# Kernel optimization log

Measured on AMD Instinct MI355X. Metric: run time of the kernel, lower is better.

## Reference

```python
import jax, jax.numpy as jnp
import numpy as np

N_CLOUDS = 16
N_PTS = 2048
K = 5            # spline kernel_size per dim
KC = K ** 3      # 125 kernel weights
BITS = np.array([[i & 1, (i >> 1) & 1, (i >> 2) & 1] for i in range(8)])  # degree-1 B-spline corners


def _radius_edges_np(pos, batch, r, max_nb=32):
    # brute-force radius graph, up to max_nb nearest neighbors within r, no self loops
    srcs, tgts = [], []
    for c in np.unique(batch):
        ids = np.where(batch == c)[0]
        P = pos[ids]
        D = np.linalg.norm(P[:, None, :] - P[None, :, :], axis=-1).astype(np.float32)
        np.fill_diagonal(D, np.inf)
        D[D > r] = np.inf
        order = np.argsort(D, axis=1)[:, :max_nb]
        valid = np.isfinite(np.take_along_axis(D, order, axis=1))
        tgt_loc = np.broadcast_to(np.arange(len(ids))[:, None], order.shape)
        srcs.append(ids[order[valid]])
        tgts.append(ids[tgt_loc[valid]])
    return np.concatenate(srcs).astype(np.int32), np.concatenate(tgts).astype(np.int32)


def _fps_np(pos, batch, ratio):
    out = []
    for c in np.unique(batch):
        ids = np.where(batch == c)[0]
        P = pos[ids]
        m = int(round(ratio * len(ids)))
        sel = [0]
        d = np.linalg.norm(P - P[0], axis=1)
        for _ in range(m - 1):
            i = int(d.argmax())
            sel.append(i)
            d = np.minimum(d, np.linalg.norm(P - P[i], axis=1))
        out.append(ids[np.array(sel)])
    return np.concatenate(out).astype(np.int32)


def setup_inputs() -> dict:
    rng = np.random.default_rng(0)
    pos = rng.random((N_CLOUDS * N_PTS, 3)).astype(np.float32)
    batch = np.repeat(np.arange(N_CLOUDS), N_PTS).astype(np.int32)

    src1, tgt1 = _radius_edges_np(pos, batch, 0.2)
    idx1 = _fps_np(pos, batch, 0.5)
    pos2, batch2 = pos[idx1], batch[idx1]
    src2, tgt2 = _radius_edges_np(pos2, batch2, 0.4)
    idx2 = _fps_np(pos2, batch2, 0.25)
    pos3, batch3 = pos2[idx2], batch2[idx2]
    src3, tgt3 = _radius_edges_np(pos3, batch3, 1.0)

    def p(shape, scale=0.1):
        return (rng.standard_normal(shape) * scale).astype(np.float32)

    inp = {
        'pos': jnp.asarray(pos), 'batch': jnp.asarray(batch),
        'src1': jnp.asarray(src1), 'tgt1': jnp.asarray(tgt1),
        'src2': jnp.asarray(src2), 'tgt2': jnp.asarray(tgt2),
        'src3': jnp.asarray(src3), 'tgt3': jnp.asarray(tgt3),
        'idx1': jnp.asarray(idx1), 'idx2': jnp.asarray(idx2),
        'W1': jnp.asarray(p((KC, 1, 64))),  'R1': jnp.asarray(p((1, 64))),   'b1': jnp.zeros((64,), jnp.float32),
        'W2': jnp.asarray(p((KC, 64, 64))), 'R2': jnp.asarray(p((64, 64))),  'b2': jnp.zeros((64,), jnp.float32),
        'W3': jnp.asarray(p((KC, 64, 128))),'R3': jnp.asarray(p((64, 128))), 'b3': jnp.zeros((128,), jnp.float32),
        'lw1': jnp.asarray(p((128, 256))), 'lb1': jnp.zeros((256,), jnp.float32),
        'lw2': jnp.asarray(p((256, 256))), 'lb2': jnp.zeros((256,), jnp.float32),
        'lw3': jnp.asarray(p((256, 10))),  'lb3': jnp.zeros((10,), jnp.float32),
    }
    return inp


def _pseudo(pos, src, tgt, r):
    return jnp.clip((pos[tgt] - pos[src]) / (2.0 * r) + 0.5, 0.0, 1.0)


def _spline_conv(x, pseudo, src, tgt, n, W, R, b):
    # SplineConv: degree-1 open B-spline basis, mean aggregation, root weight + bias
    Cin = x.shape[1]
    v = pseudo * (K - 1)                  # [E,3]
    bot = jnp.floor(v)
    frac = v - bot                        # [E,3]
    boti = bot.astype(jnp.int32)
    xj = x[src]                           # [E,Cin]
    A = jnp.zeros((n * KC, Cin), x.dtype)
    for s in range(8):                    # 8 nonzero basis products per edge
        bits = BITS[s]
        w = jnp.where(bits == 1, frac, 1.0 - frac).prod(-1)     # [E]
        idx = jnp.clip(boti + bits, 0, K - 1)                   # [E,3]
        wi = idx[:, 0] + K * idx[:, 1] + K * K * idx[:, 2]      # [E]
        A = A.at[tgt * KC + wi].add(w[:, None] * xj)
    A = A.reshape(n, KC, Cin)             # per-node per-kernel accumulated features
    msg = jnp.einsum('nkc,kco->no', A, W)
    deg = jax.ops.segment_sum(jnp.ones(tgt.shape[0], x.dtype), tgt, num_segments=n)
    msg = msg / jnp.maximum(deg, 1.0)[:, None]
    return msg + x @ R + b


def reference(pos, batch, src1, tgt1, src2, tgt2, src3, tgt3, idx1, idx2,
              W1, R1, b1, W2, R2, b2, W3, R3, b3,
              lw1, lb1, lw2, lb2, lw3, lb3):
    n1 = pos.shape[0]
    x = jnp.ones((n1, 1), pos.dtype)
    x = jax.nn.elu(_spline_conv(x, _pseudo(pos, src1, tgt1, 0.2), src1, tgt1, n1, W1, R1, b1))
    x, pos2 = x[idx1], pos[idx1]
    n2 = pos2.shape[0]
    x = jax.nn.elu(_spline_conv(x, _pseudo(pos2, src2, tgt2, 0.4), src2, tgt2, n2, W2, R2, b2))
    x, pos3 = x[idx2], pos2[idx2]
    n3 = pos3.shape[0]
    x = jax.nn.elu(_spline_conv(x, _pseudo(pos3, src3, tgt3, 1.0), src3, tgt3, n3, W3, R3, b3))
    batch3 = batch[idx1][idx2]
    num = jax.ops.segment_sum(x, batch3, num_segments=N_CLOUDS)
    cnt = jax.ops.segment_sum(jnp.ones(n3, x.dtype), batch3, num_segments=N_CLOUDS)
    g = num / jnp.maximum(cnt, 1.0)[:, None]          # global_mean_pool [16,128]
    h = jax.nn.elu(g @ lw1 + lb1)
    h = jax.nn.elu(h @ lw2 + lb2)
    # dropout is identity in eval mode
    logits = h @ lw3 + lb3
    return jax.nn.log_softmax(logits, axis=-1)
```

## Files before the change

kernel.cpp:

```cpp
#include <hip/hip_runtime.h>
#include <hip/hip_bf16.h>
#include <math.h>

#define KDIM 5
#define KC 125
#define KPAD 8192
#define EPB 32
#define NSPLIT 4
#define LDA 72
#define SSTR 40
#define XSTR 40
#define H1STR 40
#define MAXCHUNK 8192

typedef short bf16x8 __attribute__((ext_vector_type(8)));
typedef float f32x4 __attribute__((ext_vector_type(4)));

__device__ __forceinline__ float elu_f(float x) { return x > 0.f ? x : (expf(x) - 1.f); }

__device__ __forceinline__ void fadd_atomic(float* p, float v) {
    unsafeAtomicAdd(p, v);
}

__device__ __forceinline__ unsigned short f2bf(float x) {
    union { float f; unsigned u; } v; v.f = x;
    unsigned r = (v.u + 0x7FFFu + ((v.u >> 16) & 1u)) >> 16;
    return (unsigned short)r;
}

__device__ __forceinline__ void rowptr_seg(const int* __restrict__ tgt, int E, int n,
                                           int* __restrict__ rowptr, int e)
{
    if (e < E) {
        int t = tgt[e];
        int p = (e == 0) ? -1 : tgt[e - 1];
        for (int v = p + 1; v <= t; v++) rowptr[v] = e;
    } else {
        int p = tgt[E - 1];
        for (int v = p + 1; v <= n; v++) rowptr[v] = E;
    }
}

__device__ __forceinline__ void slots_seg(const float* __restrict__ posL,
                                          const int* __restrict__ src,
                                          const int* __restrict__ tgt, float rinv2,
                                          int sinkrow, unsigned* __restrict__ slots, int e)
{
    int s = src[e], t = tgt[e];
    float p0 = fminf(fmaxf((posL[t*3+0] - posL[s*3+0]) * rinv2 + 0.5f, 0.f), 1.f);
    float p1 = fminf(fmaxf((posL[t*3+1] - posL[s*3+1]) * rinv2 + 0.5f, 0.f), 1.f);
    float p2 = fminf(fmaxf((posL[t*3+2] - posL[s*3+2]) * rinv2 + 0.5f, 0.f), 1.f);
    float v0 = p0 * (KDIM - 1), v1 = p1 * (KDIM - 1), v2 = p2 * (KDIM - 1);
    int b0 = (int)floorf(v0), b1 = (int)floorf(v1), b2 = (int)floorf(v2);
    float f0 = v0 - (float)b0, f1 = v1 - (float)b1, f2 = v2 - (float)b2;
    unsigned out[8];
    #pragma unroll
    for (int sb = 0; sb < 8; sb++) {
        int i0 = sb & 1, i1 = (sb >> 1) & 1, i2 = (sb >> 2) & 1;
        float w = (i0 ? f0 : 1.f - f0) * (i1 ? f1 : 1.f - f1) * (i2 ? f2 : 1.f - f2);
        int k0 = min(b0 + i0, KDIM - 1), k1 = min(b1 + i1, KDIM - 1), k2 = min(b2 + i2, KDIM - 1);
        int wi = k0 + KDIM * k1 + KDIM * KDIM * k2;
        if (w == 0.f) wi = sinkrow;
        out[sb] = (__float_as_uint(w) & ~127u) | (unsigned)wi;
    }
    uint4* dst = (uint4*)&slots[(size_t)e * 8];
    dst[0] = make_uint4(out[0], out[1], out[2], out[3]);
    dst[1] = make_uint4(out[4], out[5], out[6], out[7]);
}

__global__ void pre1_kernel(const float* __restrict__ pos, const int* __restrict__ idx1,
                            const int* __restrict__ idx2, int n2, int n3,
                            float* __restrict__ pos2, float* __restrict__ pos3,
                            float* __restrict__ gz )
{
    int i = blockIdx.x * blockDim.x + threadIdx.x;
    int w0 = n2 * 3, w1 = w0 + n3 * 3, w2 = w1 + 16 * 128 + 16;
    if (i < w0) {
        int r = i / 3, d = i - r * 3;
        pos2[i] = pos[idx1[r] * 3 + d];
    } else if (i < w1) {
        int j = i - w0;
        int r = j / 3, d = j - r * 3;
        pos3[j] = pos[idx1[idx2[r]] * 3 + d];
    } else if (i < w2) {
        gz[i - w1] = 0.f;
    }
}

__global__ void pre2_kernel(
    const int* __restrict__ tgt1, int E1, int n1, int* __restrict__ rp1,
    const int* __restrict__ tgt2, int E2, int n2, int* __restrict__ rp2,
    const int* __restrict__ tgt3, int E3, int n3, int* __restrict__ rp3,
    const float* __restrict__ pos,  const int* __restrict__ src1, unsigned* __restrict__ slots1,
    const float* __restrict__ pos2, const int* __restrict__ src2, unsigned* __restrict__ slots2,
    const float* __restrict__ pos3, const int* __restrict__ src3, unsigned* __restrict__ slots3,
    const int* __restrict__ batch, const int* __restrict__ idx1, const int* __restrict__ idx2,
    int* __restrict__ cid, float* __restrict__ cnt)
{
    int i = blockIdx.x * blockDim.x + threadIdx.x;
    int e0 = E1 + 1, e1 = e0 + E2 + 1, e2 = e1 + E3 + 1;
    int e3 = e2 + E1, e4 = e3 + E2, e5 = e4 + E3;
    int e6 = e5 + n3;
    if (i < e0)      rowptr_seg(tgt1, E1, n1, rp1, i);
    else if (i < e1) rowptr_seg(tgt2, E2, n2, rp2, i - e0);
    else if (i < e2) rowptr_seg(tgt3, E3, n3, rp3, i - e1);
    else if (i < e3) slots_seg(pos,  src1, tgt1, 2.5f,  126, slots1, i - e2);
    else if (i < e4) slots_seg(pos2, src2, tgt2, 1.25f, 125, slots2, i - e3);
    else if (i < e5) slots_seg(pos3, src3, tgt3, 0.5f,  125, slots3, i - e4);
    else if (i < e6) {
        int j = i - e5;
        int cl = batch[idx1[idx2[j]]];
        cid[j] = cl;
        int lane = threadIdx.x & 63;
        #pragma unroll
        for (int c = 0; c < 16; c++) {
            unsigned long long m = __ballot(cl == c);
            if (m != 0ULL && lane == __ffsll((long long)m) - 1)
                fadd_atomic(&cnt[c], (float)__popcll(m));
        }
    }
}

__global__ __launch_bounds__(256) void wtT_kernel(
    const float* __restrict__ W, const float* __restrict__ R,
    int COUT, int kpad, int krows, int cin, int ntiles_k,
    unsigned short* __restrict__ WfT)
{
    __shared__ unsigned short L[64 * 65];
    int bt = blockIdx.x;
    int kt = (bt % ntiles_k) * 64;
    int nt = (bt / ntiles_k) * 64;
    int t = threadIdx.x;
    int ncol = t & 63, rowgrp = t >> 6;
    #pragma unroll
    for (int j = 0; j < 16; j++) {
        int row = j * 4 + rowgrp;
        int k = kt + row;
        int n = nt + ncol;
        float v = 0.f;
        if (k < krows) v = W[(size_t)k * COUT + n];
        else if (k < krows + cin) v = R[(size_t)(k - krows) * COUT + n];
        L[row * 65 + ncol] = f2bf(v);
    }
    __syncthreads();
    int n = nt + (t >> 2);
    int k0 = (t & 3) * 16;
    __attribute__((aligned(16))) unsigned short tmp[16];
    #pragma unroll
    for (int j = 0; j < 16; j++) tmp[j] = L[(k0 + j) * 65 + (t >> 2)];
    *(uint4*)&WfT[(size_t)n * kpad + kt + k0]     = *(uint4*)&tmp[0];
    *(uint4*)&WfT[(size_t)n * kpad + kt + k0 + 8] = *(uint4*)&tmp[8];
}

__global__ __launch_bounds__(256) void histo1_kernel(const unsigned* __restrict__ slots,
                                                     const int* __restrict__ rowptr,
                                                     unsigned short* __restrict__ Aout)
{
    __shared__ __attribute__((aligned(16))) unsigned short S[4][128 * H1STR];
    int wave = threadIdx.x >> 6, lane = threadIdx.x & 63;
    int node = blockIdx.x * 4 + wave;
    int rs = rowptr[node], re = rowptr[node + 1];
    int deg = re - rs;
    unsigned short* Sw = S[wave];

    for (int i = lane; i < 128 * H1STR / 8; i += 64)
        ((uint4*)Sw)[i] = make_uint4(0, 0, 0, 0);

    int wbase = lane * 4;
    if (wbase < deg * 8) {
        uint4 sw = *(const uint4*)&slots[(size_t)rs * 8 + wbase];
        unsigned wd[4] = {sw.x, sw.y, sw.z, sw.w};
        #pragma unroll
        for (int j = 0; j < 4; j++) {
            int e = (wbase + j) >> 3;
            int wi = wd[j] & 127u;
            Sw[wi * H1STR + e] = f2bf(__uint_as_float(wd[j] & ~127u));
        }
    }
    __syncthreads();

    const short one = 0x3F80;
    bf16x8 bones = {one, one, one, one, one, one, one, one};
    int fr = lane & 15, fq = (lane >> 4) * 8;
    f32x4 acc[8];
    #pragma unroll
    for (int tl = 0; tl < 8; tl++) {
        bf16x8 af = *(const bf16x8*)&Sw[(tl * 16 + fr) * H1STR + fq];
        acc[tl] = __builtin_amdgcn_mfma_f32_16x16x32_bf16(
            af, bones, (f32x4){0.f, 0.f, 0.f, 0.f}, 0, 0, 0);
    }

    float invdeg = 1.f / fmaxf((float)deg, 1.f);
    if ((lane & 15) == 0) {
        int rbase = (lane >> 4) * 4;
        #pragma unroll
        for (int tl = 0; tl < 8; tl++)
            #pragma unroll
            for (int r = 0; r < 4; r++) {
                int row = tl * 16 + rbase + r;
                float v = (row < KC) ? acc[tl][r] * invdeg : (row == KC ? 1.f : 0.f);
                Sw[row] = f2bf(v);
            }
    }
    __syncthreads();
    unsigned lo = Sw[2 * lane], hi = Sw[2 * lane + 1];
    ((unsigned*)(Aout + (size_t)node * 128))[lane] = lo | (hi << 16);
}

__global__ __launch_bounds__(256) void buildA_kernel(
    const unsigned* __restrict__ slots, const int* __restrict__ src,
    const int* __restrict__ rowptr, const unsigned short* __restrict__ xbf,
    int nodeBase, unsigned short* __restrict__ Aout)
{
    __shared__ __attribute__((aligned(16))) unsigned short BUF[8192];
    __shared__ int Es[EPB];
    unsigned short* S  = BUF;
    unsigned short* XT = BUF + 128 * SSTR;
    int node = nodeBase + blockIdx.x;
    int t = threadIdx.x;
    int rs = rowptr[node], re = rowptr[node + 1];
    int ne = re - rs;
    int wave = t >> 6, lane = t & 63;
    int fr = lane & 15, fq = (lane >> 4) * 8;
    int quad = lane >> 4;

    for (int i = t; i < (128 * SSTR + 64 * XSTR) / 8; i += 256)
        ((uint4*)BUF)[i] = make_uint4(0, 0, 0, 0);
    if (t < ne) Es[t] = src[rs + t];
    __syncthreads();
    if (t < ne * 8) {
        int e = t >> 3;
        unsigned word = slots[(size_t)rs * 8 + t];
        int wi = word & 127u;
        S[wi * SSTR + e] = f2bf(__uint_as_float(word & ~127u));
    }
    for (int i = t; i < ne * 64; i += 256) {
        int c = i & 63, el = i >> 6;
        XT[c * XSTR + el] = xbf[(size_t)Es[el] * 64 + c];
    }
    __syncthreads();

    f32x4 acc[2][4];
    #pragma unroll
    for (int i = 0; i < 2; i++)
        #pragma unroll
        for (int j = 0; j < 4; j++) acc[i][j] = (f32x4){0.f, 0.f, 0.f, 0.f};
    #pragma unroll
    for (int i = 0; i < 2; i++) {
        bf16x8 af = *(const bf16x8*)&S[((2 * wave + i) * 16 + fr) * SSTR + fq];
        #pragma unroll
        for (int j = 0; j < 4; j++) {
            bf16x8 bg = *(const bf16x8*)&XT[(j * 16 + fr) * XSTR + fq];
            acc[i][j] = __builtin_amdgcn_mfma_f32_16x16x32_bf16(af, bg, acc[i][j], 0, 0, 0);
        }
    }
    __syncthreads();

    float invdeg = 1.f / fmaxf((float)ne, 1.f);
    #pragma unroll
    for (int i = 0; i < 2; i++) {
        int wibase = (2 * wave + i) * 16 + quad * 4;
        #pragma unroll
        for (int r = 0; r < 4; r++) {
            int wi = wibase + r;
            if (wi < KC) {
                #pragma unroll
                for (int j = 0; j < 4; j++)
                    BUF[wi * 64 + j * 16 + fr] = f2bf(acc[i][j][r] * invdeg);
            }
        }
    }
    if (t < 64) BUF[8000 + t] = xbf[(size_t)node * 64 + t];
    else if (t < 192) BUF[8000 + t] = 0;
    __syncthreads();

    uint4* out4 = (uint4*)(Aout + (size_t)blockIdx.x * KPAD);
    const uint4* b4 = (const uint4*)BUF;
    #pragma unroll
    for (int k = 0; k < 4; k++) out4[t + k * 256] = b4[t + k * 256];
}

__global__ __launch_bounds__(256) void gemm_kernel(const unsigned short* __restrict__ A,
                                                   const unsigned short* __restrict__ BT,
                                                   int Mrows, int COUT, int Ksz, int lda,
                                                   float* __restrict__ P)
{
    __shared__ __attribute__((aligned(16))) unsigned short As[2 * 64 * LDA];
    __shared__ __attribute__((aligned(16))) unsigned short Bs[2 * 64 * LDA];
    int t = threadIdx.x;
    int mblk = blockIdx.x * 64, nblk = blockIdx.y * 64;
    int kBase = blockIdx.z * Ksz;

    int lr = t >> 2;
    int lc = (t & 3) * 16;

    const unsigned short* Ap = A + (size_t)(mblk + lr) * lda + kBase + lc;
    const unsigned short* Bp = BT + (size_t)(nblk + lr) * lda + kBase + lc;

    uint4 a0 = *(const uint4*)Ap;  uint4 a1 = *(const uint4*)(Ap + 8);
    uint4 b0 = *(const uint4*)Bp;  uint4 b1 = *(const uint4*)(Bp + 8);

    int wave = t >> 6, lane = t & 63;
    int mw = (wave & 1) * 32, nw = (wave >> 1) * 32;
    int fr = lane & 15;
    int fq = (lane >> 4) * 8;

    f32x4 acc[2][2];
    #pragma unroll
    for (int i = 0; i < 2; i++)
        #pragma unroll
        for (int j = 0; j < 2; j++) acc[i][j] = (f32x4){0.f, 0.f, 0.f, 0.f};

    *(uint4*)&As[lr * LDA + lc]     = a0;
    *(uint4*)&As[lr * LDA + lc + 8] = a1;
    *(uint4*)&Bs[lr * LDA + lc]     = b0;
    *(uint4*)&Bs[lr * LDA + lc + 8] = b1;
    __syncthreads();

    int ktiles = Ksz / 64;
    for (int kt = 0; kt < ktiles; kt++) {
        int cur = (kt & 1) * 64 * LDA;
        if (kt + 1 < ktiles) {
            Ap += 64; Bp += 64;
            a0 = *(const uint4*)Ap; a1 = *(const uint4*)(Ap + 8);
            b0 = *(const uint4*)Bp; b1 = *(const uint4*)(Bp + 8);
        }
        #pragma unroll
        for (int ks = 0; ks < 2; ks++) {
            bf16x8 af0 = *(const bf16x8*)&As[cur + (mw + fr) * LDA + ks * 32 + fq];
            bf16x8 af1 = *(const bf16x8*)&As[cur + (mw + 16 + fr) * LDA + ks * 32 + fq];
            bf16x8 bg0 = *(const bf16x8*)&Bs[cur + (nw + fr) * LDA + ks * 32 + fq];
            bf16x8 bg1 = *(const bf16x8*)&Bs[cur + (nw + 16 + fr) * LDA + ks * 32 + fq];
            acc[0][0] = __builtin_amdgcn_mfma_f32_16x16x32_bf16(af0, bg0, acc[0][0], 0, 0, 0);
            acc[0][1] = __builtin_amdgcn_mfma_f32_16x16x32_bf16(af0, bg1, acc[0][1], 0, 0, 0);
            acc[1][0] = __builtin_amdgcn_mfma_f32_16x16x32_bf16(af1, bg0, acc[1][0], 0, 0, 0);
            acc[1][1] = __builtin_amdgcn_mfma_f32_16x16x32_bf16(af1, bg1, acc[1][1], 0, 0, 0);
        }
        if (kt + 1 < ktiles) {
            int nxt = ((kt + 1) & 1) * 64 * LDA;
            *(uint4*)&As[nxt + lr * LDA + lc]     = a0;
            *(uint4*)&As[nxt + lr * LDA + lc + 8] = a1;
            *(uint4*)&Bs[nxt + lr * LDA + lc]     = b0;
            *(uint4*)&Bs[nxt + lr * LDA + lc + 8] = b1;
        }
        __syncthreads();
    }
    float* Pz = P + (size_t)blockIdx.z * Mrows * COUT;
    int crow = (lane >> 4) * 4, ccol = lane & 15;
    #pragma unroll
    for (int i = 0; i < 2; i++)
        #pragma unroll
        for (int j = 0; j < 2; j++) {
            int m0 = mblk + mw + i * 16 + crow;
            int n0 = nblk + nw + j * 16 + ccol;
            #pragma unroll
            for (int r = 0; r < 4; r++)
                Pz[(size_t)(m0 + r) * COUT + n0] = acc[i][j][r];
        }
}

__global__ void combine_kernel(const float* __restrict__ P, const float* __restrict__ b,
                               int Mrows, int COUT, int NS, float* __restrict__ xout)
{
    int i = blockIdx.x * blockDim.x + threadIdx.x;
    int total = Mrows * COUT;
    if (i >= total) return;
    float s = 0.f;
    for (int z = 0; z < NS; z++) s += P[(size_t)z * total + i];
    int o = i % COUT;
    xout[i] = elu_f(s + b[o]);
}

__global__ void combine1g_kernel(const float* __restrict__ P, const float* __restrict__ b,
                                 const int* __restrict__ idx1, int n2,
                                 unsigned short* __restrict__ x2in)
{
    int i = blockIdx.x * blockDim.x + threadIdx.x;
    if (i >= n2 * 64) return;
    int r = i >> 6, c = i & 63;
    x2in[i] = f2bf(elu_f(P[(size_t)idx1[r] * 64 + c] + b[c]));
}

__global__ void combinepool_kernel(const float* __restrict__ P, const float* __restrict__ b,
                                   const int* __restrict__ cid, int cs, int Mrows, int NS,
                                   float* __restrict__ gnum)
{
    int i = blockIdx.x * blockDim.x + threadIdx.x;
    int total = Mrows * 128;
    if (i >= total) return;
    int r = i >> 7, c = i & 127;
    float s = 0.f;
    for (int z = 0; z < NS; z++) s += P[(size_t)z * total + i];
    float v = elu_f(s + b[c]);
    fadd_atomic(&gnum[cid[cs + r] * 128 + c], v);
}

__global__ void xgather_kernel(const float* __restrict__ x_src, const int* __restrict__ idx,
                               int n, unsigned short* __restrict__ x_dst)
{
    int tid = blockIdx.x * blockDim.x + threadIdx.x;
    if (tid >= n * 64) return;
    int i = tid >> 6, c = tid & 63;
    x_dst[tid] = f2bf(x_src[(size_t)idx[i] * 64 + c]);
}

__global__ void mlp_kernel(const float* __restrict__ gnum, const float* __restrict__ cnt,
                           const float* __restrict__ lw1, const float* __restrict__ lb1,
                           const float* __restrict__ lw2, const float* __restrict__ lb2,
                           const float* __restrict__ lw3, const float* __restrict__ lb3,
                           float* __restrict__ out)
{
    __shared__ float gv[128], h1[256], h2[256], lg[10];
    __shared__ float lse_s;
    int cl = blockIdx.x, t = threadIdx.x;
    if (t < 128) gv[t] = gnum[cl * 128 + t] / fmaxf(cnt[cl], 1.f);
    __syncthreads();
    float a = lb1[t];
    for (int c = 0; c < 128; c++) a += gv[c] * lw1[c * 256 + t];
    h1[t] = elu_f(a);
    __syncthreads();
    a = lb2[t];
    for (int c = 0; c < 256; c++) a += h1[c] * lw2[c * 256 + t];
    h2[t] = elu_f(a);
    __syncthreads();
    if (t < 10) {
        a = lb3[t];
        for (int c = 0; c < 256; c++) a += h2[c] * lw3[c * 10 + t];
        lg[t] = a;
    }
    __syncthreads();
    if (t == 0) {
        float m = -1e30f;
        for (int i = 0; i < 10; i++) m = fmaxf(m, lg[i]);
        float s = 0.f;
        for (int i = 0; i < 10; i++) s += expf(lg[i] - m);
        lse_s = m + logf(s);
    }
    __syncthreads();
    if (t < 10) out[cl * 10 + t] = lg[t] - lse_s;
}

extern "C" void kernel_launch(void* const* d_in, const int* in_sizes, int n_in,
                              void* d_out, int out_size, void* d_ws, size_t ws_size,
                              hipStream_t stream)
{
    const float* pos   = (const float*)d_in[0];
    const int*   batch = (const int*)d_in[1];
    const int*   src1  = (const int*)d_in[2];
    const int*   tgt1  = (const int*)d_in[3];
    const int*   src2  = (const int*)d_in[4];
    const int*   tgt2  = (const int*)d_in[5];
    const int*   src3  = (const int*)d_in[6];
    const int*   tgt3  = (const int*)d_in[7];
    const int*   idx1  = (const int*)d_in[8];
    const int*   idx2  = (const int*)d_in[9];
    const float* W1 = (const float*)d_in[10];
    const float* R1 = (const float*)d_in[11];
    const float* b1 = (const float*)d_in[12];
    const float* W2 = (const float*)d_in[13];
    const float* R2 = (const float*)d_in[14];
    const float* b2 = (const float*)d_in[15];
    const float* W3 = (const float*)d_in[16];
    const float* R3 = (const float*)d_in[17];
    const float* b3 = (const float*)d_in[18];
    const float* lw1 = (const float*)d_in[19];
    const float* lb1 = (const float*)d_in[20];
    const float* lw2 = (const float*)d_in[21];
    const float* lb2 = (const float*)d_in[22];
    const float* lw3 = (const float*)d_in[23];
    const float* lb3 = (const float*)d_in[24];

    int n1 = in_sizes[0] / 3;
    int E1 = in_sizes[2];
    int E2 = in_sizes[4];
    int E3 = in_sizes[6];
    int n2 = in_sizes[8];
    int n3 = in_sizes[9];

    float* ws = (float*)d_ws;
    float* x2o  = ws;
    float* pos2 = x2o  + (size_t)n2 * 64;
    float* pos3 = pos2 + (size_t)n2 * 3;
    float* gnum = pos3 + (size_t)n3 * 3;
    float* cnt  = gnum + 16 * 128;
    int*   cid  = (int*)(cnt + 16);
    unsigned short* x2in = (unsigned short*)(cid + ((n3 + 4) & ~3));
    unsigned short* x3in = x2in + (size_t)n2 * 64;
    unsigned short* WfT1 = x3in + (size_t)n3 * 64;
    unsigned short* WfT2 = WfT1 + (size_t)64 * 128;
    unsigned short* WfT3 = WfT2 + (size_t)64 * KPAD;
    int*   rp1  = (int*)(WfT3 + (size_t)128 * KPAD);
    int*   rp2  = rp1 + ((n1 + 4) & ~3);
    int*   rp3  = rp2 + ((n2 + 4) & ~3);
    unsigned* slots1 = (unsigned*)(rp3 + ((n3 + 4) & ~3));
    unsigned* slots2 = slots1 + (size_t)E1 * 8;
    unsigned* slots3 = slots2 + (size_t)E2 * 8;
    unsigned short* A1buf = (unsigned short*)(slots3 + (size_t)E3 * 8);
    float*  P    = (float*)(A1buf + (size_t)n1 * 128);
    unsigned short* Abuf = (unsigned short*)(P + (size_t)8 * 1024 * 1024);

    size_t usedBytes = (size_t)((char*)Abuf - (char*)ws);
    size_t availBytes = ws_size > usedBytes ? ws_size - usedBytes : 0;
    int maxRows = (int)(availBytes / ((size_t)KPAD * 2));
    maxRows &= ~63;
    if (maxRows < 64) maxRows = 64;
    if (maxRows > MAXCHUNK) maxRows = MAXCHUNK;
    int rowsP2 = ((8 * 1024 * 1024) / (NSPLIT * 64)) & ~63;
    int rowsP3 = ((8 * 1024 * 1024) / (NSPLIT * 128)) & ~63;
    int rows2 = min(min(maxRows, rowsP2), n2);
    int rows3 = min(min(maxRows, rowsP3), n3);

    float* out = (float*)d_out;
    int Ksz = KPAD / NSPLIT;

    {
        int tot1 = n2 * 3 + n3 * 3 + 16 * 128 + 16;
        pre1_kernel<<<(tot1 + 255) / 256, 256, 0, stream>>>(pos, idx1, idx2, n2, n3,
                                                            pos2, pos3, gnum);
        int tot2 = (E1 + 1) + (E2 + 1) + (E3 + 1) + E1 + E2 + E3 + n3;
        pre2_kernel<<<(tot2 + 255) / 256, 256, 0, stream>>>(
            tgt1, E1, n1, rp1, tgt2, E2, n2, rp2, tgt3, E3, n3, rp3,
            pos,  src1, slots1, pos2, src2, slots2, pos3, src3, slots3,
            batch, idx1, idx2, cid, cnt);
        wtT_kernel<<<2, 256, 0, stream>>>(W1, R1, 64, 128, KC, 1, 2, WfT1);
        wtT_kernel<<<128, 256, 0, stream>>>(W2, R2, 64, KPAD, KC * 64, 64, KPAD / 64, WfT2);
        wtT_kernel<<<256, 256, 0, stream>>>(W3, R3, 128, KPAD, KC * 64, 64, KPAD / 64, WfT3);
    }

    histo1_kernel<<<n1 / 4, 256, 0, stream>>>(slots1, rp1, A1buf);
    {
        dim3 g1(n1 / 64, 1, 1);
        gemm_kernel<<<g1, 256, 0, stream>>>(A1buf, WfT1, n1, 64, 128, 128, P);
        combine1g_kernel<<<(n2 * 64 + 255) / 256, 256, 0, stream>>>(P, b1, idx1, n2, x2in);
    }

    for (int cs = 0; cs < n2; cs += rows2) {
        int cr = min(rows2, n2 - cs);
        buildA_kernel<<<cr, 256, 0, stream>>>(slots2, src2, rp2, x2in, cs, Abuf);
        dim3 grid(cr / 64, 1, NSPLIT);
        gemm_kernel<<<grid, 256, 0, stream>>>(Abuf, WfT2, cr, 64, Ksz, KPAD, P);
        combine_kernel<<<(cr * 64 + 255) / 256, 256, 0, stream>>>(P, b2, cr, 64, NSPLIT,
                                                                  x2o + (size_t)cs * 64);
    }
    xgather_kernel<<<(n3 * 64 + 255) / 256, 256, 0, stream>>>(x2o, idx2, n3, x3in);

    for (int cs = 0; cs < n3; cs += rows3) {
        int cr = min(rows3, n3 - cs);
        buildA_kernel<<<cr, 256, 0, stream>>>(slots3, src3, rp3, x3in, cs, Abuf);
        dim3 grid(cr / 64, 2, NSPLIT);
        gemm_kernel<<<grid, 256, 0, stream>>>(Abuf, WfT3, cr, 128, Ksz, KPAD, P);
        combinepool_kernel<<<(cr * 128 + 255) / 256, 256, 0, stream>>>(P, b3, cid, cs, cr,
                                                                       NSPLIT, gnum);
    }

    mlp_kernel<<<16, 256, 0, stream>>>(gnum, cnt, lw1, lb1, lw2, lb2, lw3, lb3, out);
}
```

Before: 368.0 us.

## Enlarge GEMM tile to 128x64 per block and double split-K factor

The bf16 MFMA GEMM now computes a 128-row by 64-column tile per block, with each wave owning 32 rows across all 64 columns, so each B fragment loaded from shared memory is reused across more MFMAs. Split-K rises from 4 to 8 to keep enough blocks in flight now that each block covers twice the rows. Chunk sizes are rounded to multiples of 128 to match. The cost is more shared memory and accumulator registers per block, plus more partial sums for the combine kernels to read. Row counts must now be multiples of 128, otherwise tail rows would be skipped.

After: 374.9 us. Within noise of the previous version (+1.9%).

```diff
diff --git a/kernel.cpp b/kernel.cpp
--- a/kernel.cpp
+++ b/kernel.cpp
@@ -6,7 +6,7 @@
 #define KC 125
 #define KPAD 8192
 #define EPB 32
-#define NSPLIT 4
+#define NSPLIT 8
 #define LDA 72
 #define SSTR 40
 #define XSTR 40
@@ -285,63 +285,77 @@
                                                    int Mrows, int COUT, int Ksz, int lda,
                                                    float* __restrict__ P)
 {
-    __shared__ __attribute__((aligned(16))) unsigned short As[2 * 64 * LDA];
+    __shared__ __attribute__((aligned(16))) unsigned short As[2 * 128 * LDA];
     __shared__ __attribute__((aligned(16))) unsigned short Bs[2 * 64 * LDA];
     int t = threadIdx.x;
-    int mblk = blockIdx.x * 64, nblk = blockIdx.y * 64;
+    int mblk = blockIdx.x * 128, nblk = blockIdx.y * 64;
     int kBase = blockIdx.z * Ksz;
 
-    int lr = t >> 2;
-    int lc = (t & 3) * 16;
-
-    const unsigned short* Ap = A + (size_t)(mblk + lr) * lda + kBase + lc;
-    const unsigned short* Bp = BT + (size_t)(nblk + lr) * lda + kBase + lc;
-
-    uint4 a0 = *(const uint4*)Ap;  uint4 a1 = *(const uint4*)(Ap + 8);
-    uint4 b0 = *(const uint4*)Bp;  uint4 b1 = *(const uint4*)(Bp + 8);
+    int ar = t >> 1, ac = (t & 1) * 32;
+    int br = t >> 2, bc = (t & 3) * 16;
+
+    const unsigned short* Ap = A + (size_t)(mblk + ar) * lda + kBase + ac;
+    const unsigned short* Bp = BT + (size_t)(nblk + br) * lda + kBase + bc;
+
+    uint4 a0 = *(const uint4*)Ap;        uint4 a1 = *(const uint4*)(Ap + 8);
+    uint4 a2 = *(const uint4*)(Ap + 16); uint4 a3 = *(const uint4*)(Ap + 24);
+    uint4 b0 = *(const uint4*)Bp;        uint4 b1 = *(const uint4*)(Bp + 8);
 
     int wave = t >> 6, lane = t & 63;
-    int mw = (wave & 1) * 32, nw = (wave >> 1) * 32;
+    int mw = wave * 32;
     int fr = lane & 15;
     int fq = (lane >> 4) * 8;
 
-    f32x4 acc[2][2];
+    f32x4 acc[2][4];
     #pragma unroll
     for (int i = 0; i < 2; i++)
         #pragma unroll
-        for (int j = 0; j < 2; j++) acc[i][j] = (f32x4){0.f, 0.f, 0.f, 0.f};
-
-    *(uint4*)&As[lr * LDA + lc]     = a0;
-    *(uint4*)&As[lr * LDA + lc + 8] = a1;
-    *(uint4*)&Bs[lr * LDA + lc]     = b0;
-    *(uint4*)&Bs[lr * LDA + lc + 8] = b1;
+        for (int j = 0; j < 4; j++) acc[i][j] = (f32x4){0.f, 0.f, 0.f, 0.f};
+
+    *(uint4*)&As[ar * LDA + ac]      = a0;
+    *(uint4*)&As[ar * LDA + ac + 8]  = a1;
+    *(uint4*)&As[ar * LDA + ac + 16] = a2;
+    *(uint4*)&As[ar * LDA + ac + 24] = a3;
+    *(uint4*)&Bs[br * LDA + bc]      = b0;
+    *(uint4*)&Bs[br * LDA + bc + 8]  = b1;
     __syncthreads();
 
     int ktiles = Ksz / 64;
     for (int kt = 0; kt < ktiles; kt++) {
-        int cur = (kt & 1) * 64 * LDA;
+        int curA = (kt & 1) * 128 * LDA;
+        int curB = (kt & 1) * 64 * LDA;
         if (kt + 1 < ktiles) {
             Ap += 64; Bp += 64;
-            a0 = *(const uint4*)Ap; a1 = *(const uint4*)(Ap + 8);
-            b0 = *(const uint4*)Bp; b1 = *(const uint4*)(Bp + 8);
+            a0 = *(const uint4*)Ap;        a1 = *(const uint4*)(Ap + 8);
+            a2 = *(const uint4*)(Ap + 16); a3 = *(const uint4*)(Ap + 24);
+            b0 = *(const uint4*)Bp;        b1 = *(const uint4*)(Bp + 8);
         }
         #pragma unroll
         for (int ks = 0; ks < 2; ks++) {
-            bf16x8 af0 = *(const bf16x8*)&As[cur + (mw + fr) * LDA + ks * 32 + fq];
-            bf16x8 af1 = *(const bf16x8*)&As[cur + (mw + 16 + fr) * LDA + ks * 32 + fq];
-            bf16x8 bg0 = *(const bf16x8*)&Bs[cur + (nw + fr) * LDA + ks * 32 + fq];
-            bf16x8 bg1 = *(const bf16x8*)&Bs[cur + (nw + 16 + fr) * LDA + ks * 32 + fq];
+            bf16x8 af0 = *(const bf16x8*)&As[curA + (mw + fr) * LDA + ks * 32 + fq];
+            bf16x8 af1 = *(const bf16x8*)&As[curA + (mw + 16 + fr) * LDA + ks * 32 + fq];
+            bf16x8 bg0 = *(const bf16x8*)&Bs[curB + (fr) * LDA + ks * 32 + fq];
+            bf16x8 bg1 = *(const bf16x8*)&Bs[curB + (16 + fr) * LDA + ks * 32 + fq];
+            bf16x8 bg2 = *(const bf16x8*)&Bs[curB + (32 + fr) * LDA + ks * 32 + fq];
+            bf16x8 bg3 = *(const bf16x8*)&Bs[curB + (48 + fr) * LDA + ks * 32 + fq];
             acc[0][0] = __builtin_amdgcn_mfma_f32_16x16x32_bf16(af0, bg0, acc[0][0], 0, 0, 0);
             acc[0][1] = __builtin_amdgcn_mfma_f32_16x16x32_bf16(af0, bg1, acc[0][1], 0, 0, 0);
+            acc[0][2] = __builtin_amdgcn_mfma_f32_16x16x32_bf16(af0, bg2, acc[0][2], 0, 0, 0);
+            acc[0][3] = __builtin_amdgcn_mfma_f32_16x16x32_bf16(af0, bg3, acc[0][3], 0, 0, 0);
             acc[1][0] = __builtin_amdgcn_mfma_f32_16x16x32_bf16(af1, bg0, acc[1][0], 0, 0, 0);
             acc[1][1] = __builtin_amdgcn_mfma_f32_16x16x32_bf16(af1, bg1, acc[1][1], 0, 0, 0);
+            acc[1][2] = __builtin_amdgcn_mfma_f32_16x16x32_bf16(af1, bg2, acc[1][2], 0, 0, 0);
+            acc[1][3] = __builtin_amdgcn_mfma_f32_16x16x32_bf16(af1, bg3, acc[1][3], 0, 0, 0);
         }
         if (kt + 1 < ktiles) {
-            int nxt = ((kt + 1) & 1) * 64 * LDA;
-            *(uint4*)&As[nxt + lr * LDA + lc]     = a0;
-            *(uint4*)&As[nxt + lr * LDA + lc + 8] = a1;
-            *(uint4*)&Bs[nxt + lr * LDA + lc]     = b0;
-            *(uint4*)&Bs[nxt + lr * LDA + lc + 8] = b1;
+            int nxtA = ((kt + 1) & 1) * 128 * LDA;
+            int nxtB = ((kt + 1) & 1) * 64 * LDA;
+            *(uint4*)&As[nxtA + ar * LDA + ac]      = a0;
+            *(uint4*)&As[nxtA + ar * LDA + ac + 8]  = a1;
+            *(uint4*)&As[nxtA + ar * LDA + ac + 16] = a2;
+            *(uint4*)&As[nxtA + ar * LDA + ac + 24] = a3;
+            *(uint4*)&Bs[nxtB + br * LDA + bc]      = b0;
+            *(uint4*)&Bs[nxtB + br * LDA + bc + 8]  = b1;
         }
         __syncthreads();
     }
@@ -350,9 +364,9 @@
     #pragma unroll
     for (int i = 0; i < 2; i++)
         #pragma unroll
-        for (int j = 0; j < 2; j++) {
+        for (int j = 0; j < 4; j++) {
             int m0 = mblk + mw + i * 16 + crow;
-            int n0 = nblk + nw + j * 16 + ccol;
+            int n0 = nblk + j * 16 + ccol;
             #pragma unroll
             for (int r = 0; r < 4; r++)
                 Pz[(size_t)(m0 + r) * COUT + n0] = acc[i][j][r];
@@ -502,11 +516,11 @@
     size_t usedBytes = (size_t)((char*)Abuf - (char*)ws);
     size_t availBytes = ws_size > usedBytes ? ws_size - usedBytes : 0;
     int maxRows = (int)(availBytes / ((size_t)KPAD * 2));
-    maxRows &= ~63;
-    if (maxRows < 64) maxRows = 64;
+    maxRows &= ~127;
+    if (maxRows < 128) maxRows = 128;
     if (maxRows > MAXCHUNK) maxRows = MAXCHUNK;
-    int rowsP2 = ((8 * 1024 * 1024) / (NSPLIT * 64)) & ~63;
-    int rowsP3 = ((8 * 1024 * 1024) / (NSPLIT * 128)) & ~63;
+    int rowsP2 = ((8 * 1024 * 1024) / (NSPLIT * 64)) & ~127;
+    int rowsP3 = ((8 * 1024 * 1024) / (NSPLIT * 128)) & ~127;
     int rows2 = min(min(maxRows, rowsP2), n2);
     int rows3 = min(min(maxRows, rowsP3), n3);
 
@@ -529,7 +543,7 @@
 
     histo1_kernel<<<n1 / 4, 256, 0, stream>>>(slots1, rp1, A1buf);
     {
-        dim3 g1(n1 / 64, 1, 1);
+        dim3 g1(n1 / 128, 1, 1);
         gemm_kernel<<<g1, 256, 0, stream>>>(A1buf, WfT1, n1, 64, 128, 128, P);
         combine1g_kernel<<<(n2 * 64 + 255) / 256, 256, 0, stream>>>(P, b1, idx1, n2, x2in);
     }
@@ -537,7 +551,7 @@
     for (int cs = 0; cs < n2; cs += rows2) {
         int cr = min(rows2, n2 - cs);
         buildA_kernel<<<cr, 256, 0, stream>>>(slots2, src2, rp2, x2in, cs, Abuf);
-        dim3 grid(cr / 64, 1, NSPLIT);
+        dim3 grid(cr / 128, 1, NSPLIT);
         gemm_kernel<<<grid, 256, 0, stream>>>(Abuf, WfT2, cr, 64, Ksz, KPAD, P);
         combine_kernel<<<(cr * 64 + 255) / 256, 256, 0, stream>>>(P, b2, cr, 64, NSPLIT,
                                                                   x2o + (size_t)cs * 64);
@@ -547,7 +561,7 @@
     for (int cs = 0; cs < n3; cs += rows3) {
         int cr = min(rows3, n3 - cs);
         buildA_kernel<<<cr, 256, 0, stream>>>(slots3, src3, rp3, x3in, cs, Abuf);
-        dim3 grid(cr / 64, 2, NSPLIT);
+        dim3 grid(cr / 128, 2, NSPLIT);
         gemm_kernel<<<grid, 256, 0, stream>>>(Abuf, WfT3, cr, 128, Ksz, KPAD, P);
         combinepool_kernel<<<(cr * 128 + 255) / 256, 256, 0, stream>>>(P, b3, cid, cs, cr,
                                                                        NSPLIT, gnum);
```
